# Optimization experiments

Measured on AMD Instinct MI355X. Metric: run time of the kernel, lower is better.

The kernel has to match this reference:

```python
import jax, jax.numpy as jnp
import numpy as np

# Static config (KITTI PointPillars-style)
B, PB, N = 4, 12000, 32          # batches, pillars per batch, max points per pillar
P = B * PB
NX, NY, NZ, F = 432, 496, 1, 64  # grid and PFN output channels
PX, PY, PZ = 0.16, 0.16, 4.0     # pillar size
XO, YO, ZO = 0.08, -39.6, -1.0   # pillar-center offsets = size/2 + range_min
EPS = 1e-3                        # BatchNorm eps


def setup_inputs() -> dict:
    key = jax.random.key(0)
    ks = jax.random.split(key, 10)
    pillars = jax.random.normal(ks[0], (P, N, 8), jnp.float32)
    # unique BEV cells per batch so the scatter (torch advanced-index assign) is well-defined
    rng = np.random.default_rng(0)
    cs = []
    for b in range(B):
        lin = rng.choice(NY * NX, size=PB, replace=False)
        cs.append(np.stack([np.full(PB, b), np.zeros(PB, np.int64), lin // NX, lin % NX], 1))
    coords = jnp.asarray(np.concatenate(cs, 0), jnp.int32)  # [P,4] = (batch, z, y, x)
    num_points = jax.random.randint(ks[1], (P,), 1, N + 1, jnp.int32)

    def bn_stats(k, f):  # rows: gamma, beta, running_mean, running_var
        k1, k2, k3, k4 = jax.random.split(k, 4)
        return jnp.stack([jax.random.uniform(k1, (f,), jnp.float32, 0.8, 1.2),
                          jax.random.normal(k2, (f,)) * 0.1,
                          jax.random.normal(k3, (f,)) * 0.1,
                          jax.random.uniform(k4, (f,), jnp.float32, 0.5, 1.5)])

    return {
        'pillars': pillars,
        'w1': jax.random.normal(ks[2], (10, F), jnp.float32) * 0.1,
        'bn1': bn_stats(ks[4], F),
        'w2': jax.random.normal(ks[3], (8, F), jnp.float32) * 0.1,
        'bn2': bn_stats(ks[5], F),
        'wf1': jax.random.normal(ks[6], (F,), jnp.float32) * 0.1,
        'wf2': jax.random.normal(ks[7], (F,), jnp.float32) * 0.1,
        'fbn1': bn_stats(ks[8], 1)[:, 0],
        'fbn2': bn_stats(ks[9], 1)[:, 0],
        'coords': coords,
        'num_points': num_points,
    }


def _bn(x, stats):  # x [..., F], stats [4, F] or [4]
    g, b, m, v = stats[0], stats[1], stats[2], stats[3]
    return (x - m) * (g * jax.lax.rsqrt(v + EPS)) + b


def _pfn(x, w, stats):  # x [P, N, C] -> [P, F]: linear + BN(eval) + relu + max over points
    h = jnp.einsum('pnc,cf->pnf', x, w)
    return jax.nn.relu(_bn(h, stats)).max(axis=1)


def _forward(pillars, w1, bn1, w2, bn2, wf1, wf2, fbn1, fbn2, coords, num_points):
    xyz = pillars[:, :, :3]                                   # [P, N, 3]
    # relative xyz to cluster mean
    mean_xyz = xyz.sum(axis=1, keepdims=True) / num_points.astype(jnp.float32)[:, None, None]
    to_cluster = xyz - mean_xyz
    # relative xyz to pillar center; coords cols = (batch, z, y, x)
    cf = coords.astype(jnp.float32)
    center = jnp.stack([cf[:, 3] * PX + XO, cf[:, 2] * PY + YO, cf[:, 1] * PZ + ZO], axis=-1)
    to_center = xyz - center[:, None, :]

    pv_in = jnp.concatenate([pillars[:, :, :4], to_cluster, to_center], axis=-1)  # [P, N, 10]
    f1 = _pfn(pv_in, w1, bn1)      # [P, F] geometric stream
    f2 = _pfn(pillars, w2, bn2)    # [P, F] seg stream (full 8 channels)

    # scatter pillar features to BEV canvas: idx = z + y*nx + x (nz=1 -> z=0)
    lin = coords[:, 1] + coords[:, 2] * NX + coords[:, 3]
    b_idx = coords[:, 0]
    bev1 = jnp.zeros((B, NZ * NY * NX, F), jnp.float32).at[b_idx, lin].set(f1)
    bev2 = jnp.zeros((B, NZ * NY * NX, F), jnp.float32).at[b_idx, lin].set(f2)
    x1 = bev1.reshape(B, NY, NX, F).transpose(0, 3, 1, 2)  # [B, F, NY, NX]
    x2 = bev2.reshape(B, NY, NX, F).transpose(0, 3, 1, 2)

    # attentional fusion: 1x1 conv (no bias) + BN2d(1) per stream, softmax over the 2 weights
    s1 = _bn(jnp.einsum('bfyx,f->byx', x1, wf1), fbn1)
    s2 = _bn(jnp.einsum('bfyx,f->byx', x2, wf2), fbn2)
    aw = jax.nn.softmax(jnp.stack([s1, s2], axis=1), axis=1)  # [B, 2, NY, NX]
    return x1 * aw[:, 0:1] + x2 * aw[:, 1:2]


def reference(pillars, w1, bn1, w2, bn2, wf1, wf2, fbn1, fbn2, coords, num_points):
    return _forward(pillars, w1, bn1, w2, bn2, wf1, wf2, fbn1, fbn2, coords, num_points)
```

## Files before the change

kernel.cpp:

```cpp
#include <hip/hip_runtime.h>
#include <math.h>

#define NXC 432
#define NYC 496
#define CELLS (NYC * NXC)
#define BATCH 4
#define PTOT 48000
#define EPSC 1e-3f
#define TCELLS 128

typedef float f2v    __attribute__((ext_vector_type(2)));
typedef float f4v    __attribute__((ext_vector_type(4)));
typedef float f32x16 __attribute__((ext_vector_type(16)));
typedef __bf16 bf16x8 __attribute__((ext_vector_type(8)));
typedef unsigned int u32x2 __attribute__((ext_vector_type(2)));
typedef unsigned int u32x4 __attribute__((ext_vector_type(4)));


__device__ __forceinline__ unsigned int pk_bf16(float a, float b) {
    __bf16 ha = (__bf16)a, hb = (__bf16)b;
    unsigned short ua = __builtin_bit_cast(unsigned short, ha);
    unsigned short ub = __builtin_bit_cast(unsigned short, hb);
    return ((unsigned int)ub << 16) | ua;
}

__global__ __launch_bounds__(64) void fold_kernel(
    const float* __restrict__ w1, const float* __restrict__ bn1,
    const float* __restrict__ w2, const float* __restrict__ bn2,
    const float* __restrict__ wf1, const float* __restrict__ wf2,
    unsigned int* __restrict__ tbl)
{
    const int c = threadIdx.x;
    const float s1 = bn1[c] * rsqrtf(bn1[192 + c] + EPSC);
    const float w10 = w1[c],       w11 = w1[64 + c],  w12 = w1[128 + c];
    const float w13 = w1[192 + c], w14 = w1[256 + c], w15 = w1[320 + c];
    const float w16 = w1[384 + c], w17 = w1[448 + c], w18 = w1[512 + c];
    const float w19 = w1[576 + c];
    const float AX = (w10 + w14 + w17) * s1;
    const float AY = (w11 + w15 + w18) * s1;
    const float AZ = (w12 + w16 + w19) * s1;
    const float AI = w13 * s1;

    const float s2 = bn2[c] * rsqrtf(bn2[192 + c] + EPSC);
    float B[8];
#pragma unroll
    for (int k = 0; k < 8; ++k) B[k] = w2[k * 64 + c] * s2;

    ((u32x2*)tbl)[c]         = (u32x2){pk_bf16(AX, AY), pk_bf16(AZ, AI)};
    ((u32x4*)(tbl + 128))[c] = (u32x4){pk_bf16(B[0], B[1]), pk_bf16(B[2], B[3]),
                                       pk_bf16(B[4], B[5]), pk_bf16(B[6], B[7])};
    ((f4v*)(tbl + 384))[c]   = (f4v){bn1[64 + c] - bn1[128 + c] * s1,
                                     w14 * s1, w15 * s1, w16 * s1};
    ((f4v*)(tbl + 640))[c]   = (f4v){w17 * s1, w18 * s1, w19 * s1,
                                     bn2[64 + c] - bn2[128 + c] * s2};
    ((f2v*)(tbl + 896))[c]   = (f2v){wf1[c], wf2[c]};
}

__global__ __launch_bounds__(256) void pfe_kernel(
    const float* __restrict__ pillars, const unsigned int* __restrict__ tbl,
    const float* __restrict__ fbn1, const float* __restrict__ fbn2,
    const int* __restrict__ coords, const int* __restrict__ num_points,
    float* __restrict__ comb, int* __restrict__ map)
{
    const int tid  = threadIdx.x;
    const int lane = tid & 63;
    const int ln   = lane & 31;
    const bool hi  = lane >= 32;
    const int p = __builtin_amdgcn_readfirstlane(blockIdx.x * 4 + (tid >> 6));
    const float* __restrict__ pl = pillars + (size_t)p * 256;

    const f4v v0 = *(const f4v*)(pl + ln * 8);
    const f4v v1 = *(const f4v*)(pl + ln * 8 + 4);

    float sx = v0.x, sy = v0.y, sz = v0.z;
#pragma unroll
    for (int off = 1; off <= 16; off <<= 1) {
        sx += __shfl_xor(sx, off);
        sy += __shfl_xor(sy, off);
        sz += __shfl_xor(sz, off);
    }
    const float inv_np = 1.0f / (float)num_points[p];
    const float mxm = sx * inv_np, mym = sy * inv_np, mzm = sz * inv_np;

    const int c1 = coords[p * 4 + 1], c2 = coords[p * 4 + 2], c3 = coords[p * 4 + 3];
    const float cx = c3 * 0.16f + 0.08f;
    const float cy = c2 * 0.16f + (-39.6f);
    const float cz = c1 * 4.0f  + (-1.0f);

    const u32x2* At = (const u32x2*)tbl;
    const u32x4* Bt = (const u32x4*)(tbl + 128);
    const f4v*   Ct = (const f4v*)(tbl + 384);
    const f4v*   Dt = (const f4v*)(tbl + 640);
    const f2v*   Et = (const f2v*)(tbl + 896);

    bf16x8 bfr1[2], bfr2[2];
    float C0c[2], C2c[2], WF1c[2], WF2c[2];
#pragma unroll
    for (int i = 0; i < 2; ++i) {
        const int c = ln + i * 32;
        const u32x2 a2 = At[c];
        const u32x4 w1v = {a2.x, a2.y, 0u, 0u};
        bfr1[i] = __builtin_bit_cast(bf16x8, w1v);
        bfr2[i] = __builtin_bit_cast(bf16x8, Bt[c]);
        const f4v k0 = Ct[c];
        const f4v k1 = Dt[c];
        const f2v wfp = Et[c];
        C0c[i] = k0.x - (mxm * k0.y + mym * k0.z + mzm * k0.w)
                      - (cx * k1.x + cy * k1.y + cz * k1.z);
        C2c[i] = k1.w;
        WF1c[i] = wfp.x;
        WF2c[i] = wfp.y;
    }

    bf16x8 a;
    {
        const float f[8] = {v0.x, v0.y, v0.z, v0.w, v1.x, v1.y, v1.z, v1.w};
#pragma unroll
        for (int e = 0; e < 8; ++e) {
            const __bf16 h = (__bf16)f[e];
            const __bf16 l = (__bf16)(f[e] - (float)h);
            a[e] = hi ? l : h;
        }
    }

    f32x16 d0 = {0.f}, d1 = {0.f}, d2 = {0.f}, d3 = {0.f};
    d0 = __builtin_amdgcn_mfma_f32_32x32x16_bf16(a, bfr1[0], d0, 0, 0, 0);
    d1 = __builtin_amdgcn_mfma_f32_32x32x16_bf16(a, bfr1[1], d1, 0, 0, 0);
    d2 = __builtin_amdgcn_mfma_f32_32x32x16_bf16(a, bfr2[0], d2, 0, 0, 0);
    d3 = __builtin_amdgcn_mfma_f32_32x32x16_bf16(a, bfr2[1], d3, 0, 0, 0);

    float m0 = d0[0], m1 = d1[0], m2 = d2[0], m3 = d3[0];
#pragma unroll
    for (int r = 1; r < 16; ++r) {
        m0 = fmaxf(m0, d0[r]); m1 = fmaxf(m1, d1[r]);
        m2 = fmaxf(m2, d2[r]); m3 = fmaxf(m3, d3[r]);
    }
    m0 = fmaxf(m0, __shfl_xor(m0, 32));
    m1 = fmaxf(m1, __shfl_xor(m1, 32));
    m2 = fmaxf(m2, __shfl_xor(m2, 32));
    m3 = fmaxf(m3, __shfl_xor(m3, 32));

    const float f1A = fmaxf(m0 + C0c[0], 0.f);
    const float f1B = fmaxf(m1 + C0c[1], 0.f);
    const float f2A = fmaxf(m2 + C2c[0], 0.f);
    const float f2B = fmaxf(m3 + C2c[1], 0.f);

    float dd1 = f1A * WF1c[0] + f1B * WF1c[1];
    float dd2 = f2A * WF2c[0] + f2B * WF2c[1];
#pragma unroll
    for (int off = 1; off <= 16; off <<= 1) {
        dd1 += __shfl_xor(dd1, off);
        dd2 += __shfl_xor(dd2, off);
    }
    const float sc1 = (dd1 - fbn1[2]) * (fbn1[0] * rsqrtf(fbn1[3] + EPSC)) + fbn1[1];
    const float sc2 = (dd2 - fbn2[2]) * (fbn2[0] * rsqrtf(fbn2[3] + EPSC)) + fbn2[1];
    const float a0 = 1.0f / (1.0f + expf(sc2 - sc1));

    if (!hi) {
        comb[p * 64 + ln]      = fmaf(f1A - f2A, a0, f2A);
        comb[p * 64 + 32 + ln] = fmaf(f1B - f2B, a0, f2B);
    }
    if (lane == 0) {
        const int lin = c1 + c2 * NXC + c3;
        map[coords[p * 4 + 0] * CELLS + lin] = p;
    }
}

__global__ __launch_bounds__(256) void emit_kernel(
    const int* __restrict__ map, const float* __restrict__ comb,
    float* __restrict__ out)
{
    __shared__ float lds[64 * 132];
    __shared__ int mcell[128];
    const int t = threadIdx.x;
    const int gbase = blockIdx.x * TCELLS;

    {
        const int c = t >> 1;
        const int h = (t & 1) * 32;
        const int m = map[gbase + c];
        if ((t & 1) == 0) mcell[c] = m;
        if (m >= 0) {
            const float* src = comb + (size_t)m * 64 + h;
            float* dst = lds + h * 132 + c;
#pragma unroll
            for (int j = 0; j < 8; j++) {
                const float4 v = *(const float4*)(src + j * 4);
                dst[(j * 4 + 0) * 132] = v.x;
                dst[(j * 4 + 1) * 132] = v.y;
                dst[(j * 4 + 2) * 132] = v.z;
                dst[(j * 4 + 3) * 132] = v.w;
            }
        }
    }
    __syncthreads();

    const int b = gbase / CELLS;
    const int L = gbase - b * CELLS;
    float* obase = out + (size_t)(b * 64) * CELLS + L;
#pragma unroll
    for (int r = 0; r < 8; r++) {
        const int idx = r * 256 + t;
        const int f = idx >> 5;
        const int g = idx & 31;
        const int4 mg = *(const int4*)&mcell[g * 4];
        f4v v = {0.f, 0.f, 0.f, 0.f};
        if ((mg.x & mg.y & mg.z & mg.w) >= 0) {
            const f4v w = *(const f4v*)(lds + f * 132 + g * 4);
            v.x = (mg.x < 0) ? 0.f : w.x;
            v.y = (mg.y < 0) ? 0.f : w.y;
            v.z = (mg.z < 0) ? 0.f : w.z;
            v.w = (mg.w < 0) ? 0.f : w.w;
        }
        __builtin_nontemporal_store(v, (f4v*)(obase + (size_t)f * CELLS + g * 4));
    }
}

extern "C" void kernel_launch(void* const* d_in, const int* in_sizes, int n_in,
                              void* d_out, int out_size, void* d_ws, size_t ws_size,
                              hipStream_t stream) {
    const float* pillars = (const float*)d_in[0];
    const float* w1      = (const float*)d_in[1];
    const float* bn1     = (const float*)d_in[2];
    const float* w2      = (const float*)d_in[3];
    const float* bn2     = (const float*)d_in[4];
    const float* wf1     = (const float*)d_in[5];
    const float* wf2     = (const float*)d_in[6];
    const float* fbn1    = (const float*)d_in[7];
    const float* fbn2    = (const float*)d_in[8];
    const int*   coords  = (const int*)d_in[9];
    const int*   nump    = (const int*)d_in[10];
    float* out = (float*)d_out;

    int*   map  = (int*)d_ws;
    float* comb = (float*)((char*)d_ws + (size_t)BATCH * CELLS * 4);
    unsigned int* tbl = (unsigned int*)((char*)d_ws + (size_t)BATCH * CELLS * 4
                                        + (size_t)PTOT * 64 * 4);

    (void)hipMemsetAsync(map, 0xFF, (size_t)BATCH * CELLS * 4, stream);
    fold_kernel<<<1, 64, 0, stream>>>(w1, bn1, w2, bn2, wf1, wf2, tbl);
    pfe_kernel<<<PTOT / 4, 256, 0, stream>>>(pillars, tbl, fbn1, fbn2,
                                             coords, nump, comb, map);
    emit_kernel<<<(BATCH * CELLS) / TCELLS, 256, 0, stream>>>(map, comb, out);
}
```

Measured before the change: 86.24 us.

## Process four pillars per wavefront and use plain stores in emit

Each wavefront now handles four pillars instead of one. It loads all four pillars' points and coords up front, and reuses the folded weight tables and fusion BN constants loaded once per wave. The grid shrinks by a factor of four. The max reduction becomes a tree to shorten dependency chains. The emit kernel's nontemporal stores become ordinary stores. The trade-off is fewer waves, so less latency hiding across waves, and higher register pressure from four pillars in flight.

Measured after the change: 78.71 us (median of 2 runs). 8.7% less time.

```diff
diff --git a/kernel.cpp b/kernel.cpp
--- a/kernel.cpp
+++ b/kernel.cpp
@@ -15,7 +15,6 @@
 typedef __bf16 bf16x8 __attribute__((ext_vector_type(8)));
 typedef unsigned int u32x2 __attribute__((ext_vector_type(2)));
 typedef unsigned int u32x4 __attribute__((ext_vector_type(4)));
-
 
 __device__ __forceinline__ unsigned int pk_bf16(float a, float b) {
     __bf16 ha = (__bf16)a, hb = (__bf16)b;
@@ -56,6 +55,17 @@
     ((f2v*)(tbl + 896))[c]   = (f2v){wf1[c], wf2[c]};
 }
 
+__device__ __forceinline__ float rmax16(const f32x16 d) {
+    const float t0 = fmaxf(fmaxf(d[0], d[1]), d[2]);
+    const float t1 = fmaxf(fmaxf(d[3], d[4]), d[5]);
+    const float t2 = fmaxf(fmaxf(d[6], d[7]), d[8]);
+    const float t3 = fmaxf(fmaxf(d[9], d[10]), d[11]);
+    const float t4 = fmaxf(fmaxf(d[12], d[13]), d[14]);
+    const float u0 = fmaxf(fmaxf(t0, t1), t2);
+    const float u1 = fmaxf(fmaxf(t3, t4), d[15]);
+    return fmaxf(u0, u1);
+}
+
 __global__ __launch_bounds__(256) void pfe_kernel(
     const float* __restrict__ pillars, const unsigned int* __restrict__ tbl,
     const float* __restrict__ fbn1, const float* __restrict__ fbn2,
@@ -66,26 +76,8 @@
     const int lane = tid & 63;
     const int ln   = lane & 31;
     const bool hi  = lane >= 32;
-    const int p = __builtin_amdgcn_readfirstlane(blockIdx.x * 4 + (tid >> 6));
-    const float* __restrict__ pl = pillars + (size_t)p * 256;
-
-    const f4v v0 = *(const f4v*)(pl + ln * 8);
-    const f4v v1 = *(const f4v*)(pl + ln * 8 + 4);
-
-    float sx = v0.x, sy = v0.y, sz = v0.z;
-#pragma unroll
-    for (int off = 1; off <= 16; off <<= 1) {
-        sx += __shfl_xor(sx, off);
-        sy += __shfl_xor(sy, off);
-        sz += __shfl_xor(sz, off);
-    }
-    const float inv_np = 1.0f / (float)num_points[p];
-    const float mxm = sx * inv_np, mym = sy * inv_np, mzm = sz * inv_np;
-
-    const int c1 = coords[p * 4 + 1], c2 = coords[p * 4 + 2], c3 = coords[p * 4 + 3];
-    const float cx = c3 * 0.16f + 0.08f;
-    const float cy = c2 * 0.16f + (-39.6f);
-    const float cz = c1 * 4.0f  + (-1.0f);
+    const int q = __builtin_amdgcn_readfirstlane(blockIdx.x * 4 + (tid >> 6));
+    const int pbase = q * 4;
 
     const u32x2* At = (const u32x2*)tbl;
     const u32x4* Bt = (const u32x4*)(tbl + 128);
@@ -94,75 +86,109 @@
     const f2v*   Et = (const f2v*)(tbl + 896);
 
     bf16x8 bfr1[2], bfr2[2];
-    float C0c[2], C2c[2], WF1c[2], WF2c[2];
-#pragma unroll
-    for (int i = 0; i < 2; ++i) {
-        const int c = ln + i * 32;
+    f4v k0c[2], k1c[2];
+    f2v wfc[2];
+#pragma unroll
+    for (int j = 0; j < 2; ++j) {
+        const int c = ln + j * 32;
         const u32x2 a2 = At[c];
         const u32x4 w1v = {a2.x, a2.y, 0u, 0u};
-        bfr1[i] = __builtin_bit_cast(bf16x8, w1v);
-        bfr2[i] = __builtin_bit_cast(bf16x8, Bt[c]);
-        const f4v k0 = Ct[c];
-        const f4v k1 = Dt[c];
-        const f2v wfp = Et[c];
-        C0c[i] = k0.x - (mxm * k0.y + mym * k0.z + mzm * k0.w)
-                      - (cx * k1.x + cy * k1.y + cz * k1.z);
-        C2c[i] = k1.w;
-        WF1c[i] = wfp.x;
-        WF2c[i] = wfp.y;
-    }
-
-    bf16x8 a;
-    {
-        const float f[8] = {v0.x, v0.y, v0.z, v0.w, v1.x, v1.y, v1.z, v1.w};
-#pragma unroll
-        for (int e = 0; e < 8; ++e) {
-            const __bf16 h = (__bf16)f[e];
-            const __bf16 l = (__bf16)(f[e] - (float)h);
-            a[e] = hi ? l : h;
-        }
-    }
-
-    f32x16 d0 = {0.f}, d1 = {0.f}, d2 = {0.f}, d3 = {0.f};
-    d0 = __builtin_amdgcn_mfma_f32_32x32x16_bf16(a, bfr1[0], d0, 0, 0, 0);
-    d1 = __builtin_amdgcn_mfma_f32_32x32x16_bf16(a, bfr1[1], d1, 0, 0, 0);
-    d2 = __builtin_amdgcn_mfma_f32_32x32x16_bf16(a, bfr2[0], d2, 0, 0, 0);
-    d3 = __builtin_amdgcn_mfma_f32_32x32x16_bf16(a, bfr2[1], d3, 0, 0, 0);
-
-    float m0 = d0[0], m1 = d1[0], m2 = d2[0], m3 = d3[0];
-#pragma unroll
-    for (int r = 1; r < 16; ++r) {
-        m0 = fmaxf(m0, d0[r]); m1 = fmaxf(m1, d1[r]);
-        m2 = fmaxf(m2, d2[r]); m3 = fmaxf(m3, d3[r]);
-    }
-    m0 = fmaxf(m0, __shfl_xor(m0, 32));
-    m1 = fmaxf(m1, __shfl_xor(m1, 32));
-    m2 = fmaxf(m2, __shfl_xor(m2, 32));
-    m3 = fmaxf(m3, __shfl_xor(m3, 32));
-
-    const float f1A = fmaxf(m0 + C0c[0], 0.f);
-    const float f1B = fmaxf(m1 + C0c[1], 0.f);
-    const float f2A = fmaxf(m2 + C2c[0], 0.f);
-    const float f2B = fmaxf(m3 + C2c[1], 0.f);
-
-    float dd1 = f1A * WF1c[0] + f1B * WF1c[1];
-    float dd2 = f2A * WF2c[0] + f2B * WF2c[1];
-#pragma unroll
-    for (int off = 1; off <= 16; off <<= 1) {
-        dd1 += __shfl_xor(dd1, off);
-        dd2 += __shfl_xor(dd2, off);
-    }
-    const float sc1 = (dd1 - fbn1[2]) * (fbn1[0] * rsqrtf(fbn1[3] + EPSC)) + fbn1[1];
-    const float sc2 = (dd2 - fbn2[2]) * (fbn2[0] * rsqrtf(fbn2[3] + EPSC)) + fbn2[1];
-    const float a0 = 1.0f / (1.0f + expf(sc2 - sc1));
-
-    if (!hi) {
-        comb[p * 64 + ln]      = fmaf(f1A - f2A, a0, f2A);
-        comb[p * 64 + 32 + ln] = fmaf(f1B - f2B, a0, f2B);
-    }
-    if (lane == 0) {
-        const int lin = c1 + c2 * NXC + c3;
-        map[coords[p * 4 + 0] * CELLS + lin] = p;
+        bfr1[j] = __builtin_bit_cast(bf16x8, w1v);
+        bfr2[j] = __builtin_bit_cast(bf16x8, Bt[c]);
+        k0c[j] = Ct[c];
+        k1c[j] = Dt[c];
+        wfc[j] = Et[c];
+    }
+    const float r1s = fbn1[0] * rsqrtf(fbn1[3] + EPSC);
+    const float r1b = fbn1[1], r1m = fbn1[2];
+    const float r2s = fbn2[0] * rsqrtf(fbn2[3] + EPSC);
+    const float r2b = fbn2[1], r2m = fbn2[2];
+
+    f4v pv0[4], pv1[4];
+    int cb[4], cc1[4], cc2[4], cc3[4];
+    float invn[4];
+#pragma unroll
+    for (int i = 0; i < 4; ++i) {
+        const float* pl = pillars + (size_t)(pbase + i) * 256;
+        pv0[i] = *(const f4v*)(pl + ln * 8);
+        pv1[i] = *(const f4v*)(pl + ln * 8 + 4);
+        cb[i]  = coords[(pbase + i) * 4 + 0];
+        cc1[i] = coords[(pbase + i) * 4 + 1];
+        cc2[i] = coords[(pbase + i) * 4 + 2];
+        cc3[i] = coords[(pbase + i) * 4 + 3];
+        invn[i] = 1.0f / (float)num_points[pbase + i];
+    }
+
+#pragma unroll
+    for (int i = 0; i < 4; ++i) {
+        const f4v v0 = pv0[i], v1 = pv1[i];
+
+        float sx = v0.x, sy = v0.y, sz = v0.z;
+#pragma unroll
+        for (int off = 1; off <= 16; off <<= 1) {
+            sx += __shfl_xor(sx, off);
+            sy += __shfl_xor(sy, off);
+            sz += __shfl_xor(sz, off);
+        }
+        const float mxm = sx * invn[i], mym = sy * invn[i], mzm = sz * invn[i];
+        const float cx = cc3[i] * 0.16f + 0.08f;
+        const float cy = cc2[i] * 0.16f + (-39.6f);
+        const float cz = cc1[i] * 4.0f  + (-1.0f);
+
+        float C0c[2];
+#pragma unroll
+        for (int j = 0; j < 2; ++j)
+            C0c[j] = k0c[j].x - (mxm * k0c[j].y + mym * k0c[j].z + mzm * k0c[j].w)
+                   - (cx * k1c[j].x + cy * k1c[j].y + cz * k1c[j].z);
+
+        bf16x8 a;
+        {
+            const float f[8] = {v0.x, v0.y, v0.z, v0.w, v1.x, v1.y, v1.z, v1.w};
+#pragma unroll
+            for (int e = 0; e < 8; ++e) {
+                const __bf16 h8 = (__bf16)f[e];
+                const __bf16 l8 = (__bf16)(f[e] - (float)h8);
+                a[e] = hi ? l8 : h8;
+            }
+        }
+
+        const f32x16 zero = {};
+        const f32x16 d0 = __builtin_amdgcn_mfma_f32_32x32x16_bf16(a, bfr1[0], zero, 0, 0, 0);
+        const f32x16 d1 = __builtin_amdgcn_mfma_f32_32x32x16_bf16(a, bfr1[1], zero, 0, 0, 0);
+        const f32x16 d2 = __builtin_amdgcn_mfma_f32_32x32x16_bf16(a, bfr2[0], zero, 0, 0, 0);
+        const f32x16 d3 = __builtin_amdgcn_mfma_f32_32x32x16_bf16(a, bfr2[1], zero, 0, 0, 0);
+
+        float m0 = rmax16(d0), m1 = rmax16(d1), m2 = rmax16(d2), m3 = rmax16(d3);
+        m0 = fmaxf(m0, __shfl_xor(m0, 32));
+        m1 = fmaxf(m1, __shfl_xor(m1, 32));
+        m2 = fmaxf(m2, __shfl_xor(m2, 32));
+        m3 = fmaxf(m3, __shfl_xor(m3, 32));
+
+        const float f1A = fmaxf(m0 + C0c[0], 0.f);
+        const float f1B = fmaxf(m1 + C0c[1], 0.f);
+        const float f2A = fmaxf(m2 + k1c[0].w, 0.f);
+        const float f2B = fmaxf(m3 + k1c[1].w, 0.f);
+
+        float dd1 = f1A * wfc[0].x + f1B * wfc[1].x;
+        float dd2 = f2A * wfc[0].y + f2B * wfc[1].y;
+#pragma unroll
+        for (int off = 1; off <= 16; off <<= 1) {
+            dd1 += __shfl_xor(dd1, off);
+            dd2 += __shfl_xor(dd2, off);
+        }
+        const float sc1 = (dd1 - r1m) * r1s + r1b;
+        const float sc2 = (dd2 - r2m) * r2s + r2b;
+        const float a0 = 1.0f / (1.0f + expf(sc2 - sc1));
+
+        const int p = pbase + i;
+        if (!hi) {
+            comb[p * 64 + ln]      = fmaf(f1A - f2A, a0, f2A);
+            comb[p * 64 + 32 + ln] = fmaf(f1B - f2B, a0, f2B);
+        }
+        if (lane == 0) {
+            const int lin = cc1[i] + cc2[i] * NXC + cc3[i];
+            map[cb[i] * CELLS + lin] = p;
+        }
     }
 }
 
@@ -212,7 +238,7 @@
             v.z = (mg.z < 0) ? 0.f : w.z;
             v.w = (mg.w < 0) ? 0.f : w.w;
         }
-        __builtin_nontemporal_store(v, (f4v*)(obase + (size_t)f * CELLS + g * 4));
+        *(f4v*)(obase + (size_t)f * CELLS + g * 4) = v;
     }
 }
 
@@ -239,7 +265,7 @@
 
     (void)hipMemsetAsync(map, 0xFF, (size_t)BATCH * CELLS * 4, stream);
     fold_kernel<<<1, 64, 0, stream>>>(w1, bn1, w2, bn2, wf1, wf2, tbl);
-    pfe_kernel<<<PTOT / 4, 256, 0, stream>>>(pillars, tbl, fbn1, fbn2,
-                                             coords, nump, comb, map);
+    pfe_kernel<<<PTOT / 16, 256, 0, stream>>>(pillars, tbl, fbn1, fbn2,
+                                              coords, nump, comb, map);
     emit_kernel<<<(BATCH * CELLS) / TCELLS, 256, 0, stream>>>(map, comb, out);
 }
```
